# Performance work log

Measured on AMD Instinct MI355X. Metric: run time of the kernel, lower is better.

## Reference

```python
import jax, jax.numpy as jnp
import numpy as np

B, S, D, H = 32, 512, 768, 12
HD = D // H
FF = 4 * D
EPS = 1e-5


def layernorm(x, g, b):
    mu = jnp.mean(x, axis=-1, keepdims=True)
    var = jnp.mean(jnp.square(x - mu), axis=-1, keepdims=True)
    return (x - mu) * jax.lax.rsqrt(var + EPS) * g + b


def setup_inputs() -> dict:
    key = jax.random.key(0)
    ks = jax.random.split(key, 10)
    s = 0.02
    return {
        "x": jax.random.normal(ks[0], (B, S, D), jnp.float32),
        "edge_bias": jax.random.normal(ks[1], (H, S, S), jnp.float32) * s,
        "ln1_g": jnp.ones((D,), jnp.float32),
        "ln1_b": jnp.zeros((D,), jnp.float32),
        "qkv_w": jax.random.normal(ks[2], (3 * D, D), jnp.float32) * s,
        "qkv_b": jnp.zeros((3 * D,), jnp.float32),
        "proj_w": jax.random.normal(ks[3], (D, D), jnp.float32) * s,
        "proj_b": jnp.zeros((D,), jnp.float32),
        "ln2_g": jnp.ones((D,), jnp.float32),
        "ln2_b": jnp.zeros((D,), jnp.float32),
        "fc1_w": jax.random.normal(ks[4], (FF, D), jnp.float32) * s,
        "fc1_b": jnp.zeros((FF,), jnp.float32),
        "fc2_w": jax.random.normal(ks[5], (D, FF), jnp.float32) * s,
        "fc2_b": jnp.zeros((D,), jnp.float32),
    }


def reference(x, edge_bias, ln1_g, ln1_b, qkv_w, qkv_b, proj_w, proj_b,
              ln2_g, ln2_b, fc1_w, fc1_b, fc2_w, fc2_b):
    shortcut = x
    xn = layernorm(x, ln1_g, ln1_b)
    # qkv: [B,S,3D] -> [3,B,H,S,HD]
    qkv = (xn @ qkv_w.T + qkv_b).reshape(B, S, 3, H, HD).transpose(2, 0, 3, 1, 4)
    q, k, v = qkv[0], qkv[1], qkv[2]
    q = q * (HD ** -0.5)
    attn = jnp.einsum('bhqd,bhkd->bhqk', q, k) + edge_bias[None]
    attn = jax.nn.softmax(attn, axis=-1)
    o = jnp.einsum('bhqk,bhkd->bhqd', attn, v)
    o = o.transpose(0, 2, 1, 3).reshape(B, S, D)
    o = o @ proj_w.T + proj_b
    x = shortcut + o
    h = layernorm(x, ln2_g, ln2_b)
    h = jax.nn.gelu(h @ fc1_w.T + fc1_b, approximate=False)
    h = h @ fc2_w.T + fc2_b
    return x + h
```

## Files before the change

kernel.cpp:

```cpp
#include <hip/hip_runtime.h>

typedef unsigned short u16;
typedef unsigned int u32;
typedef float f32x4 __attribute__((ext_vector_type(4)));
typedef __bf16 bf16x8 __attribute__((ext_vector_type(8)));

__device__ __forceinline__ u16 f2bf(float f) {
  u32 u = __float_as_uint(f);
  u += 0x7fffu + ((u >> 16) & 1u);
  return (u16)(u >> 16);
}

__device__ __forceinline__ float bf2f(u16 v) {
  return __uint_as_float((u32)v << 16);
}

__device__ __forceinline__ void gload16(const u16* g, u16* l) {
  __builtin_amdgcn_global_load_lds(
      (__attribute__((address_space(1))) void*)(u16*)g,
      (__attribute__((address_space(3))) void*)l, 16, 0, 0);
}

__global__ __launch_bounds__(256) void cvt_bf16(const float* __restrict__ in,
                                                u16* __restrict__ o, int n4) {
  int i = blockIdx.x * 256 + threadIdx.x;
  if (i >= n4) return;
  float4 f = reinterpret_cast<const float4*>(in)[i];
  u32 lo = (u32)f2bf(f.x) | ((u32)f2bf(f.y) << 16);
  u32 hi = (u32)f2bf(f.z) | ((u32)f2bf(f.w) << 16);
  reinterpret_cast<uint2*>(o)[i] = make_uint2(lo, hi);
}

__global__ __launch_bounds__(256) void cvt_w_pack(const float* __restrict__ in,
                                                  u16* __restrict__ o, int N, int K) {
  int i = blockIdx.x * 256 + threadIdx.x;
  const int ng = K >> 3;
  if (i >= N * ng) return;
  const int n = i / ng;
  const int k = (i - n * ng) * 8;
  const float4 f0 = reinterpret_cast<const float4*>(in + (size_t)n * K + k)[0];
  const float4 f1 = reinterpret_cast<const float4*>(in + (size_t)n * K + k)[1];
  u32 p0 = (u32)f2bf(f0.x) | ((u32)f2bf(f0.y) << 16);
  u32 p1 = (u32)f2bf(f0.z) | ((u32)f2bf(f0.w) << 16);
  u32 p2 = (u32)f2bf(f1.x) | ((u32)f2bf(f1.y) << 16);
  u32 p3 = (u32)f2bf(f1.z) | ((u32)f2bf(f1.w) << 16);
  u16* dst = o + ((size_t)(k >> 5) * N + n) * 32 + (k & 31);
  reinterpret_cast<uint4*>(dst)[0] = make_uint4(p0, p1, p2, p3);
}

__global__ __launch_bounds__(256) void ln_bf16(const float* __restrict__ x,
                                               const float* __restrict__ g,
                                               const float* __restrict__ b,
                                               u16* __restrict__ o) {
  const int row = blockIdx.x;
  const int t = threadIdx.x;
  const float* xr = x + (size_t)row * 768;
  float a0 = xr[t], a1 = xr[t + 256], a2 = xr[t + 512];
  float s = a0 + a1 + a2;
  float ss = a0 * a0 + a1 * a1 + a2 * a2;
#pragma unroll
  for (int m = 1; m < 64; m <<= 1) {
    s += __shfl_xor(s, m);
    ss += __shfl_xor(ss, m);
  }
  __shared__ float sb[8];
  if ((t & 63) == 0) { sb[t >> 6] = s; sb[4 + (t >> 6)] = ss; }
  __syncthreads();
  s = sb[0] + sb[1] + sb[2] + sb[3];
  ss = sb[4] + sb[5] + sb[6] + sb[7];
  const float mu = s * (1.0f / 768.0f);
  const float var = ss * (1.0f / 768.0f) - mu * mu;
  const float rs = rsqrtf(var + 1e-5f);
#pragma unroll
  for (int c = 0; c < 3; ++c) {
    const int col = t + c * 256;
    const float a = (c == 0) ? a0 : (c == 1) ? a1 : a2;
    o[((size_t)(col >> 5) * 16384 + row) * 32 + (col & 31)] =
        f2bf((a - mu) * rs * g[col] + b[col]);
  }
}

enum { EPI_QKV = 0, EPI_PROJ = 1, EPI_GELU = 2, EPI_OUT = 3 };

template <int EPI>
__global__ __launch_bounds__(512, 2) void gemm_bt(
    const u16* __restrict__ A, const u16* __restrict__ W,
    const float* __restrict__ bias, const float* __restrict__ res,
    float* __restrict__ outf, u16* __restrict__ outb,
    u16* __restrict__ outq, u16* __restrict__ outk, u16* __restrict__ outv,
    int M, int N, int K) {
  __shared__ u16 SA[4 * 8192];
  __shared__ u16 SB[4 * 8192];
  const int tid = threadIdx.x;
  const int wid = tid >> 6, l = tid & 63;
  const int wm = wid >> 2, wn = wid & 3;
  const int lg = l >> 4, lc = l & 15;

  const u32 nbn = gridDim.x;
  const u32 orig = blockIdx.y * nbn + blockIdx.x;
  const u32 cpx = (nbn * gridDim.y) >> 3;
  const u32 wgid = (orig & 7) * cpx + (orig >> 3);
  const int bn = wgid % nbn;
  const int bm = wgid / nbn;

  const size_t Msl = (size_t)M * 32;
  const size_t Nsl = (size_t)N * 32;
  const size_t lane_a = (size_t)(bm * 256 + wid * 16 + (l >> 2)) * 32 +
                        (((l & 3) ^ ((l >> 3) & 3)) << 3);
  const size_t lane_w = (size_t)(bn * 256 + wid * 16 + (l >> 2)) * 32 +
                        (((l & 3) ^ ((l >> 3) & 3)) << 3);

  const int sg = (lg ^ ((lc >> 1) & 3)) << 3;

  f32x4 acc[8][4] = {};

  const int NU = K >> 5;

#define STAGE(u)                                                      \
  {                                                                   \
    const int slot_ = (u) & 3;                                        \
    const u16* Au_ = A + (size_t)(u) * Msl + lane_a;                  \
    const u16* Wu_ = W + (size_t)(u) * Nsl + lane_w;                  \
    gload16(Au_, &SA[slot_ * 8192 + wid * 512]);                      \
    gload16(Au_ + 4096, &SA[slot_ * 8192 + 4096 + wid * 512]);        \
    gload16(Wu_, &SB[slot_ * 8192 + wid * 512]);                      \
    gload16(Wu_ + 4096, &SB[slot_ * 8192 + 4096 + wid * 512]);        \
  }

  STAGE(0);
  STAGE(1);
  STAGE(2);
  asm volatile("s_waitcnt vmcnt(8)" ::: "memory");
  __builtin_amdgcn_s_barrier();

  for (int u = 0; u < NU; ++u) {
    const u16* sa = &SA[(u & 3) * 8192];
    const u16* sb = &SB[(u & 3) * 8192];
    bf16x8 af[8], bf[4];
#pragma unroll
    for (int mi = 0; mi < 8; ++mi)
      af[mi] = *reinterpret_cast<const bf16x8*>(&sa[(wm * 128 + mi * 16 + lc) * 32 + sg]);
#pragma unroll
    for (int ni = 0; ni < 4; ++ni)
      bf[ni] = *reinterpret_cast<const bf16x8*>(&sb[(wn * 64 + ni * 16 + lc) * 32 + sg]);
    if (u + 3 < NU) STAGE(u + 3);
    __builtin_amdgcn_s_barrier();
    __builtin_amdgcn_s_setprio(1);
#pragma unroll
    for (int mi = 0; mi < 8; ++mi)
#pragma unroll
      for (int ni = 0; ni < 4; ++ni)
        acc[mi][ni] = __builtin_amdgcn_mfma_f32_16x16x32_bf16(af[mi], bf[ni], acc[mi][ni], 0, 0, 0);
    __builtin_amdgcn_s_setprio(0);
    if (u + 3 < NU) {
      asm volatile("s_waitcnt vmcnt(8)" ::: "memory");
    } else if (u + 2 < NU) {
      asm volatile("s_waitcnt vmcnt(4)" ::: "memory");
    } else if (u + 1 < NU) {
      asm volatile("s_waitcnt vmcnt(0)" ::: "memory");
    }
    __builtin_amdgcn_s_barrier();
  }
#undef STAGE

  const int rbase = bm * 256 + wm * 128;
  const int cbase = bn * 256 + wn * 64;
#pragma unroll
  for (int mi = 0; mi < 8; ++mi) {
#pragma unroll
    for (int ni = 0; ni < 4; ++ni) {
#pragma unroll
      for (int r = 0; r < 4; ++r) {
        const int i = rbase + mi * 16 + lg * 4 + r;
        const int j = cbase + ni * 16 + lc;
        float v = acc[mi][ni][r] + bias[j];
        if constexpr (EPI == EPI_QKV) {
          const int t = j / 768;
          const int rr = j - t * 768;
          const int h = rr >> 6, hd = rr & 63;
          const int bb = i >> 9, ssi = i & 511;
          if (t == 0) {
            outq[((size_t)(bb * 12 + h) * 512 + ssi) * 64 + hd] = f2bf(v * 0.125f);
          } else if (t == 1) {
            outk[((size_t)(bb * 12 + h) * 512 + ssi) * 64 + hd] = f2bf(v);
          } else {
            outv[((size_t)(bb * 12 + h) * 64 + hd) * 512 + ssi] = f2bf(v);
          }
        } else if constexpr (EPI == EPI_PROJ) {
          outf[(size_t)i * 768 + j] = v + res[(size_t)i * 768 + j];
        } else if constexpr (EPI == EPI_GELU) {
          float gl = 0.5f * v * (1.0f + erff(v * 0.70710678118654752f));
          outb[((size_t)(j >> 5) * 16384 + i) * 32 + (j & 31)] = f2bf(gl);
        } else {
          outf[(size_t)i * 768 + j] = v + res[(size_t)i * 768 + j];
        }
      }
    }
  }
}

__global__ __launch_bounds__(256) void attn_fwd(const u16* __restrict__ q,
                                                const u16* __restrict__ k,
                                                const u16* __restrict__ vt,
                                                const u16* __restrict__ ebb,
                                                u16* __restrict__ o) {
  __shared__ u16 Ks[128 * 64];
  __shared__ u16 Vs[64 * 128];
  __shared__ u16 Bs[64 * 128];
  __shared__ u16 P[4 * 1024];
  const int tid = threadIdx.x;
  const int w = tid >> 6, l = tid & 63;
  const int lg = l >> 4, lc = l & 15;
  const int xcd = blockIdx.x & 7;
  const int wg = xcd * 384 + (blockIdx.x >> 3);
  const int qt = wg & 7;
  const int b = (wg >> 3) & 31;
  const int h = wg >> 8;
  const int bh = b * 12 + h;
  const int q0 = qt * 64;
  const u16* qp = q + (size_t)bh * 512 * 64;
  const u16* kp = k + (size_t)bh * 512 * 64;
  const u16* vtp = vt + (size_t)bh * 64 * 512;
  const u16* ep = ebb + (size_t)h * 262144 + (size_t)q0 * 512;

  bf16x8 aq[2];
#pragma unroll
  for (int kk = 0; kk < 2; ++kk)
    aq[kk] = *reinterpret_cast<const bf16x8*>(qp + (q0 + w * 16 + lc) * 64 + kk * 32 + lg * 8);

  float m[4], lsum[4];
  f32x4 oa[4] = {};
#pragma unroll
  for (int r = 0; r < 4; ++r) { m[r] = -1e30f; lsum[r] = 0.f; }

  const int krow_l = l >> 3;
  const int kgr = ((l & 7) ^ (l >> 3)) << 3;
  const int vrow_l = l >> 4;
  const int vswz = 4 * (w & 1) + (l >> 4);
  const int vgr = (((l & 15) ^ vswz)) << 3;
  const int bgr = (l & 15) << 3;
  char* Pw = (char*)&P[w * 1024];

  for (int kc = 0; kc < 4; ++kc) {
    const int kb = kc * 128;
    __syncthreads();
#pragma unroll
    for (int i = 0; i < 4; ++i) {
      const int grp = i * 4 + w;
      gload16(kp + (size_t)(kb + grp * 8 + krow_l) * 64 + kgr, &Ks[grp * 512]);
      gload16(vtp + (size_t)(grp * 4 + vrow_l) * 512 + kb + vgr, &Vs[grp * 512]);
      gload16(ep + (size_t)(grp * 4 + vrow_l) * 512 + kb + bgr, &Bs[grp * 512]);
    }
    __syncthreads();

    f32x4 s[8] = {};
#pragma unroll
    for (int kt = 0; kt < 8; ++kt) {
      const int kbyte = (kt * 16 + lc) * 128;
      const int sw = lc & 7;
      bf16x8 b0 = *reinterpret_cast<const bf16x8*>((const char*)Ks + kbyte + ((lg ^ sw) << 4));
      bf16x8 b1 = *reinterpret_cast<const bf16x8*>((const char*)Ks + kbyte + (((4 + lg) ^ sw) << 4));
      s[kt] = __builtin_amdgcn_mfma_f32_16x16x32_bf16(aq[0], b0, s[kt], 0, 0, 0);
      s[kt] = __builtin_amdgcn_mfma_f32_16x16x32_bf16(aq[1], b1, s[kt], 0, 0, 0);
    }
#pragma unroll
    for (int kt = 0; kt < 8; ++kt)
#pragma unroll
      for (int r = 0; r < 4; ++r)
        s[kt][r] += bf2f(Bs[(w * 16 + lg * 4 + r) * 128 + kt * 16 + lc]);
#pragma unroll
    for (int r = 0; r < 4; ++r) {
      float mc = s[0][r];
#pragma unroll
      for (int kt = 1; kt < 8; ++kt) mc = fmaxf(mc, s[kt][r]);
      mc = fmaxf(mc, __shfl_xor(mc, 1));
      mc = fmaxf(mc, __shfl_xor(mc, 2));
      mc = fmaxf(mc, __shfl_xor(mc, 4));
      mc = fmaxf(mc, __shfl_xor(mc, 8));
      const float mn = fmaxf(m[r], mc);
      const float al = __expf(m[r] - mn);
      m[r] = mn;
      float sum = 0.f;
#pragma unroll
      for (int kt = 0; kt < 8; ++kt) {
        float pv = __expf(s[kt][r] - mn);
        s[kt][r] = pv;
        sum += pv;
      }
      sum += __shfl_xor(sum, 1);
      sum += __shfl_xor(sum, 2);
      sum += __shfl_xor(sum, 4);
      sum += __shfl_xor(sum, 8);
      lsum[r] = lsum[r] * al + sum;
#pragma unroll
      for (int ni = 0; ni < 4; ++ni) oa[ni][r] *= al;
    }
#pragma unroll
    for (int kt = 0; kt < 8; ++kt)
#pragma unroll
      for (int r = 0; r < 4; ++r) {
        const int row = lg * 4 + r;
        int byte = (row << 8) + ((kt * 16 + lc) << 1);
        byte ^= (row & 7) << 4;
        *reinterpret_cast<u16*>(Pw + byte) = f2bf(s[kt][r]);
      }
#pragma unroll
    for (int ks = 0; ks < 4; ++ks) {
      int pbyte = (lc << 8) + ks * 64 + lg * 16;
      pbyte ^= (lc & 7) << 4;
      bf16x8 pa = *reinterpret_cast<const bf16x8*>(Pw + pbyte);
#pragma unroll
      for (int ni = 0; ni < 4; ++ni) {
        const int vbyte = (ni * 16 + lc) * 256 + (((ks * 4 + lg) ^ (lc & 7)) << 4);
        bf16x8 bv = *reinterpret_cast<const bf16x8*>((const char*)Vs + vbyte);
        oa[ni] = __builtin_amdgcn_mfma_f32_16x16x32_bf16(pa, bv, oa[ni], 0, 0, 0);
      }
    }
  }

  float inv[4];
#pragma unroll
  for (int r = 0; r < 4; ++r) inv[r] = 1.0f / lsum[r];
#pragma unroll
  for (int ni = 0; ni < 4; ++ni)
#pragma unroll
    for (int r = 0; r < 4; ++r) {
      const int i = b * 512 + q0 + w * 16 + lg * 4 + r;
      const int j = h * 64 + ni * 16 + lc;
      o[((size_t)(j >> 5) * 16384 + i) * 32 + (j & 31)] = f2bf(oa[ni][r] * inv[r]);
    }
}

extern "C" void kernel_launch(void* const* d_in, const int* in_sizes, int n_in,
                              void* d_out, int out_size, void* d_ws, size_t ws_size,
                              hipStream_t stream) {
  const float* x     = (const float*)d_in[0];
  const float* ebias = (const float*)d_in[1];
  const float* ln1g  = (const float*)d_in[2];
  const float* ln1b  = (const float*)d_in[3];
  const float* qkvw  = (const float*)d_in[4];
  const float* qkvb  = (const float*)d_in[5];
  const float* projw = (const float*)d_in[6];
  const float* projb = (const float*)d_in[7];
  const float* ln2g  = (const float*)d_in[8];
  const float* ln2b  = (const float*)d_in[9];
  const float* fc1w  = (const float*)d_in[10];
  const float* fc1b  = (const float*)d_in[11];
  const float* fc2w  = (const float*)d_in[12];
  const float* fc2b  = (const float*)d_in[13];
  float* out = (float*)d_out;

  char* p = (char*)d_ws;
  const size_t ACT = (size_t)16384 * 768 * 2;
  u16* xnb = (u16*)(p);
  u16* qb  = (u16*)(p + ACT);
  u16* kb  = (u16*)(p + 2 * ACT);
  u16* vb  = (u16*)(p + 3 * ACT);
  u16* ffb = (u16*)(p + 4 * ACT);
  u16* ebb = (u16*)(p + 4 * ACT);
  float* x2 = (float*)(p + 4 * ACT + (size_t)16384 * 3072 * 2);
  char* wz = p + 4 * ACT + (size_t)16384 * 3072 * 2 + (size_t)16384 * 768 * 4;
  u16* wq  = (u16*)wz;
  u16* wp  = wq + (size_t)2304 * 768;
  u16* wf1 = wp + (size_t)768 * 768;
  u16* wf2 = wf1 + (size_t)3072 * 768;

  cvt_w_pack<<<864, 256, 0, stream>>>(qkvw, wq, 2304, 768);
  cvt_w_pack<<<288, 256, 0, stream>>>(projw, wp, 768, 768);
  cvt_w_pack<<<1152, 256, 0, stream>>>(fc1w, wf1, 3072, 768);
  cvt_w_pack<<<1152, 256, 0, stream>>>(fc2w, wf2, 768, 3072);
  cvt_bf16<<<3072, 256, 0, stream>>>(ebias, ebb, 786432);

  ln_bf16<<<16384, 256, 0, stream>>>(x, ln1g, ln1b, xnb);

  gemm_bt<EPI_QKV><<<dim3(9, 64), 512, 0, stream>>>(
      xnb, wq, qkvb, nullptr, nullptr, nullptr, qb, kb, vb, 16384, 2304, 768);

  attn_fwd<<<3072, 256, 0, stream>>>(qb, kb, vb, ebb, xnb);

  gemm_bt<EPI_PROJ><<<dim3(3, 64), 512, 0, stream>>>(
      xnb, wp, projb, x, x2, nullptr, nullptr, nullptr, nullptr, 16384, 768, 768);

  ln_bf16<<<16384, 256, 0, stream>>>(x2, ln2g, ln2b, kb);

  gemm_bt<EPI_GELU><<<dim3(12, 64), 512, 0, stream>>>(
      kb, wf1, fc1b, nullptr, nullptr, ffb, nullptr, nullptr, nullptr, 16384, 3072, 768);

  gemm_bt<EPI_OUT><<<dim3(3, 64), 512, 0, stream>>>(
      ffb, wf2, fc2b, x2, out, nullptr, nullptr, nullptr, nullptr, 16384, 768, 3072);
}
```

Measured before the change: 536.9 us.

## Split GEMM main loop into two half-phases and use tanh-approx GELU

The GEMM k-loop is split into two phases. Each phase loads half of the A fragments, issues either the A or the W prefetch for stage u+3, and runs half of the MFMAs, with an extra barrier in between. The aim is to interleave global loads and LDS reads with MFMA work so the memory pipe and the matrix units overlap more. The exact erf GELU in the FC1 epilogue is also replaced by the tanh approximation written as a sigmoid with fast exp and rcp. This changes numerics slightly and may go beyond what the reference tolerance allows.

```diff
diff --git a/kernel.cpp b/kernel.cpp
--- a/kernel.cpp
+++ b/kernel.cpp
@@ -116,20 +116,24 @@
 
   const int NU = K >> 5;
 
-#define STAGE(u)                                                      \
+#define STAGE_A(u)                                                    \
   {                                                                   \
     const int slot_ = (u) & 3;                                        \
     const u16* Au_ = A + (size_t)(u) * Msl + lane_a;                  \
-    const u16* Wu_ = W + (size_t)(u) * Nsl + lane_w;                  \
     gload16(Au_, &SA[slot_ * 8192 + wid * 512]);                      \
     gload16(Au_ + 4096, &SA[slot_ * 8192 + 4096 + wid * 512]);        \
+  }
+#define STAGE_W(u)                                                    \
+  {                                                                   \
+    const int slot_ = (u) & 3;                                        \
+    const u16* Wu_ = W + (size_t)(u) * Nsl + lane_w;                  \
     gload16(Wu_, &SB[slot_ * 8192 + wid * 512]);                      \
     gload16(Wu_ + 4096, &SB[slot_ * 8192 + 4096 + wid * 512]);        \
   }
 
-  STAGE(0);
-  STAGE(1);
-  STAGE(2);
+  STAGE_A(0); STAGE_W(0);
+  STAGE_A(1); STAGE_W(1);
+  STAGE_A(2); STAGE_W(2);
   asm volatile("s_waitcnt vmcnt(8)" ::: "memory");
   __builtin_amdgcn_s_barrier();
 
@@ -138,16 +142,29 @@
     const u16* sb = &SB[(u & 3) * 8192];
     bf16x8 af[8], bf[4];
 #pragma unroll
-    for (int mi = 0; mi < 8; ++mi)
+    for (int mi = 0; mi < 4; ++mi)
       af[mi] = *reinterpret_cast<const bf16x8*>(&sa[(wm * 128 + mi * 16 + lc) * 32 + sg]);
 #pragma unroll
     for (int ni = 0; ni < 4; ++ni)
       bf[ni] = *reinterpret_cast<const bf16x8*>(&sb[(wn * 64 + ni * 16 + lc) * 32 + sg]);
-    if (u + 3 < NU) STAGE(u + 3);
+    if (u + 3 < NU) STAGE_A(u + 3);
     __builtin_amdgcn_s_barrier();
     __builtin_amdgcn_s_setprio(1);
 #pragma unroll
-    for (int mi = 0; mi < 8; ++mi)
+    for (int mi = 0; mi < 4; ++mi)
+#pragma unroll
+      for (int ni = 0; ni < 4; ++ni)
+        acc[mi][ni] = __builtin_amdgcn_mfma_f32_16x16x32_bf16(af[mi], bf[ni], acc[mi][ni], 0, 0, 0);
+    __builtin_amdgcn_s_setprio(0);
+    __builtin_amdgcn_s_barrier();
+#pragma unroll
+    for (int mi = 4; mi < 8; ++mi)
+      af[mi] = *reinterpret_cast<const bf16x8*>(&sa[(wm * 128 + mi * 16 + lc) * 32 + sg]);
+    if (u + 3 < NU) STAGE_W(u + 3);
+    __builtin_amdgcn_s_barrier();
+    __builtin_amdgcn_s_setprio(1);
+#pragma unroll
+    for (int mi = 4; mi < 8; ++mi)
 #pragma unroll
       for (int ni = 0; ni < 4; ++ni)
         acc[mi][ni] = __builtin_amdgcn_mfma_f32_16x16x32_bf16(af[mi], bf[ni], acc[mi][ni], 0, 0, 0);
@@ -161,7 +178,8 @@
     }
     __builtin_amdgcn_s_barrier();
   }
-#undef STAGE
+#undef STAGE_A
+#undef STAGE_W
 
   const int rbase = bm * 256 + wm * 128;
   const int cbase = bn * 256 + wn * 64;
@@ -189,7 +207,8 @@
         } else if constexpr (EPI == EPI_PROJ) {
           outf[(size_t)i * 768 + j] = v + res[(size_t)i * 768 + j];
         } else if constexpr (EPI == EPI_GELU) {
-          float gl = 0.5f * v * (1.0f + erff(v * 0.70710678118654752f));
+          float z = -1.5957691216f * v - 0.07135481627f * v * v * v;
+          float gl = v * __builtin_amdgcn_rcpf(1.0f + __expf(z));
           outb[((size_t)(j >> 5) * 16384 + i) * 32 + (j & 31)] = f2bf(gl);
         } else {
           outf[(size_t)i * 768 + j] = v + res[(size_t)i * 768 + j];
```

Result: no change. 534.4 us (-0.5%).

## Shrink GEMM tiles to 128x128 with double buffering and use sigmoid-GELU approximation

Applied to the files above, without the earlier changes.

Replaces the 256x256-tile, 512-thread, 4-stage-pipelined GEMM with a 128x128-tile, 256-thread, double-buffered version. It drops the explicit vmcnt waits and priority hints, and grids are doubled in each dimension. The exact erf GELU is also swapped for a tanh-style sigmoid approximation using fast exp and rcp. Smaller tiles mean less data reuse per block and a shallower pipeline. The GELU change alters numerics slightly.

```diff
diff --git a/kernel.cpp b/kernel.cpp
--- a/kernel.cpp
+++ b/kernel.cpp
@@ -83,17 +83,17 @@
 enum { EPI_QKV = 0, EPI_PROJ = 1, EPI_GELU = 2, EPI_OUT = 3 };
 
 template <int EPI>
-__global__ __launch_bounds__(512, 2) void gemm_bt(
+__global__ __launch_bounds__(256) void gemm_bt(
     const u16* __restrict__ A, const u16* __restrict__ W,
     const float* __restrict__ bias, const float* __restrict__ res,
     float* __restrict__ outf, u16* __restrict__ outb,
     u16* __restrict__ outq, u16* __restrict__ outk, u16* __restrict__ outv,
     int M, int N, int K) {
-  __shared__ u16 SA[4 * 8192];
-  __shared__ u16 SB[4 * 8192];
+  __shared__ u16 SA[2][128 * 32];
+  __shared__ u16 SB[2][128 * 32];
   const int tid = threadIdx.x;
   const int wid = tid >> 6, l = tid & 63;
-  const int wm = wid >> 2, wn = wid & 3;
+  const int wr = wid >> 1, wc = wid & 1;
   const int lg = l >> 4, lc = l & 15;
 
   const u32 nbn = gridDim.x;
@@ -105,68 +105,53 @@
 
   const size_t Msl = (size_t)M * 32;
   const size_t Nsl = (size_t)N * 32;
-  const size_t lane_a = (size_t)(bm * 256 + wid * 16 + (l >> 2)) * 32 +
+  const size_t lane_a = (size_t)(bm * 128 + wid * 16 + (l >> 2)) * 32 +
                         (((l & 3) ^ ((l >> 3) & 3)) << 3);
-  const size_t lane_w = (size_t)(bn * 256 + wid * 16 + (l >> 2)) * 32 +
+  const size_t lane_w = (size_t)(bn * 128 + wid * 16 + (l >> 2)) * 32 +
                         (((l & 3) ^ ((l >> 3) & 3)) << 3);
-
   const int sg = (lg ^ ((lc >> 1) & 3)) << 3;
 
-  f32x4 acc[8][4] = {};
+  f32x4 acc[4][4] = {};
 
   const int NU = K >> 5;
 
-#define STAGE(u)                                                      \
-  {                                                                   \
-    const int slot_ = (u) & 3;                                        \
-    const u16* Au_ = A + (size_t)(u) * Msl + lane_a;                  \
-    const u16* Wu_ = W + (size_t)(u) * Nsl + lane_w;                  \
-    gload16(Au_, &SA[slot_ * 8192 + wid * 512]);                      \
-    gload16(Au_ + 4096, &SA[slot_ * 8192 + 4096 + wid * 512]);        \
-    gload16(Wu_, &SB[slot_ * 8192 + wid * 512]);                      \
-    gload16(Wu_ + 4096, &SB[slot_ * 8192 + 4096 + wid * 512]);        \
-  }
-
-  STAGE(0);
-  STAGE(1);
-  STAGE(2);
-  asm volatile("s_waitcnt vmcnt(8)" ::: "memory");
-  __builtin_amdgcn_s_barrier();
-
+#define STAGE(u, buf)                                             \
+  {                                                               \
+    const u16* Au_ = A + (size_t)(u) * Msl + lane_a;              \
+    const u16* Wu_ = W + (size_t)(u) * Nsl + lane_w;              \
+    gload16(Au_, &SA[buf][wid * 512]);                            \
+    gload16(Au_ + 2048, &SA[buf][2048 + wid * 512]);              \
+    gload16(Wu_, &SB[buf][wid * 512]);                            \
+    gload16(Wu_ + 2048, &SB[buf][2048 + wid * 512]);              \
+  }
+
+  STAGE(0, 0);
+  __syncthreads();
+
+  int cur = 0;
   for (int u = 0; u < NU; ++u) {
-    const u16* sa = &SA[(u & 3) * 8192];
-    const u16* sb = &SB[(u & 3) * 8192];
-    bf16x8 af[8], bf[4];
-#pragma unroll
-    for (int mi = 0; mi < 8; ++mi)
-      af[mi] = *reinterpret_cast<const bf16x8*>(&sa[(wm * 128 + mi * 16 + lc) * 32 + sg]);
+    if (u + 1 < NU) STAGE(u + 1, cur ^ 1);
+    bf16x8 af[4], bf[4];
+#pragma unroll
+    for (int mi = 0; mi < 4; ++mi)
+      af[mi] = *reinterpret_cast<const bf16x8*>(&SA[cur][(wr * 64 + mi * 16 + lc) * 32 + sg]);
 #pragma unroll
     for (int ni = 0; ni < 4; ++ni)
-      bf[ni] = *reinterpret_cast<const bf16x8*>(&sb[(wn * 64 + ni * 16 + lc) * 32 + sg]);
-    if (u + 3 < NU) STAGE(u + 3);
-    __builtin_amdgcn_s_barrier();
-    __builtin_amdgcn_s_setprio(1);
-#pragma unroll
-    for (int mi = 0; mi < 8; ++mi)
+      bf[ni] = *reinterpret_cast<const bf16x8*>(&SB[cur][(wc * 64 + ni * 16 + lc) * 32 + sg]);
+#pragma unroll
+    for (int mi = 0; mi < 4; ++mi)
 #pragma unroll
       for (int ni = 0; ni < 4; ++ni)
         acc[mi][ni] = __builtin_amdgcn_mfma_f32_16x16x32_bf16(af[mi], bf[ni], acc[mi][ni], 0, 0, 0);
-    __builtin_amdgcn_s_setprio(0);
-    if (u + 3 < NU) {
-      asm volatile("s_waitcnt vmcnt(8)" ::: "memory");
-    } else if (u + 2 < NU) {
-      asm volatile("s_waitcnt vmcnt(4)" ::: "memory");
-    } else if (u + 1 < NU) {
-      asm volatile("s_waitcnt vmcnt(0)" ::: "memory");
-    }
-    __builtin_amdgcn_s_barrier();
+    __syncthreads();
+    cur ^= 1;
   }
 #undef STAGE
 
-  const int rbase = bm * 256 + wm * 128;
-  const int cbase = bn * 256 + wn * 64;
-#pragma unroll
-  for (int mi = 0; mi < 8; ++mi) {
+  const int rbase = bm * 128 + wr * 64;
+  const int cbase = bn * 128 + wc * 64;
+#pragma unroll
+  for (int mi = 0; mi < 4; ++mi) {
 #pragma unroll
     for (int ni = 0; ni < 4; ++ni) {
 #pragma unroll
@@ -189,7 +174,8 @@
         } else if constexpr (EPI == EPI_PROJ) {
           outf[(size_t)i * 768 + j] = v + res[(size_t)i * 768 + j];
         } else if constexpr (EPI == EPI_GELU) {
-          float gl = 0.5f * v * (1.0f + erff(v * 0.70710678118654752f));
+          float z = -1.5957691216f * v - 0.07135481627f * v * v * v;
+          float gl = v * __builtin_amdgcn_rcpf(1.0f + __expf(z));
           outb[((size_t)(j >> 5) * 16384 + i) * 32 + (j & 31)] = f2bf(gl);
         } else {
           outf[(size_t)i * 768 + j] = v + res[(size_t)i * 768 + j];
@@ -373,19 +359,19 @@
 
   ln_bf16<<<16384, 256, 0, stream>>>(x, ln1g, ln1b, xnb);
 
-  gemm_bt<EPI_QKV><<<dim3(9, 64), 512, 0, stream>>>(
+  gemm_bt<EPI_QKV><<<dim3(18, 128), 256, 0, stream>>>(
       xnb, wq, qkvb, nullptr, nullptr, nullptr, qb, kb, vb, 16384, 2304, 768);
 
   attn_fwd<<<3072, 256, 0, stream>>>(qb, kb, vb, ebb, xnb);
 
-  gemm_bt<EPI_PROJ><<<dim3(3, 64), 512, 0, stream>>>(
+  gemm_bt<EPI_PROJ><<<dim3(6, 128), 256, 0, stream>>>(
       xnb, wp, projb, x, x2, nullptr, nullptr, nullptr, nullptr, 16384, 768, 768);
 
   ln_bf16<<<16384, 256, 0, stream>>>(x2, ln2g, ln2b, kb);
 
-  gemm_bt<EPI_GELU><<<dim3(12, 64), 512, 0, stream>>>(
+  gemm_bt<EPI_GELU><<<dim3(24, 128), 256, 0, stream>>>(
       kb, wf1, fc1b, nullptr, nullptr, ffb, nullptr, nullptr, nullptr, 16384, 3072, 768);
 
-  gemm_bt<EPI_OUT><<<dim3(3, 64), 512, 0, stream>>>(
+  gemm_bt<EPI_OUT><<<dim3(6, 128), 256, 0, stream>>>(
       ffb, wf2, fc2b, x2, out, nullptr, nullptr, nullptr, nullptr, 16384, 768, 3072);
 }
```

Measured after the change: 599.3 us. 11.6% more time.

## Switch GEMM to double-buffered K=64 stages and use fast GELU approximation

Applied to the files above, without the earlier changes.

Restructures the GEMM main loop from a four-slot K=32 ring with three stages in flight to a two-slot double buffer holding K=64 per stage, with one block per CU. It aims to cut barriers and waitcnt overhead per K step. In exchange it reduces prefetch depth and occupancy, which can expose global load latency. The exact erf GELU in the fc1 epilogue is also replaced by a sigmoid-based tanh approximation using fast exp and reciprocal, which changes numerics slightly.

```diff
diff --git a/kernel.cpp b/kernel.cpp
--- a/kernel.cpp
+++ b/kernel.cpp
@@ -83,14 +83,14 @@
 enum { EPI_QKV = 0, EPI_PROJ = 1, EPI_GELU = 2, EPI_OUT = 3 };
 
 template <int EPI>
-__global__ __launch_bounds__(512, 2) void gemm_bt(
+__global__ __launch_bounds__(512, 1) void gemm_bt(
     const u16* __restrict__ A, const u16* __restrict__ W,
     const float* __restrict__ bias, const float* __restrict__ res,
     float* __restrict__ outf, u16* __restrict__ outb,
     u16* __restrict__ outq, u16* __restrict__ outk, u16* __restrict__ outv,
     int M, int N, int K) {
-  __shared__ u16 SA[4 * 8192];
-  __shared__ u16 SB[4 * 8192];
+  __shared__ u16 SA[2 * 16384];
+  __shared__ u16 SB[2 * 16384];
   const int tid = threadIdx.x;
   const int wid = tid >> 6, l = tid & 63;
   const int wm = wid >> 2, wn = wid & 3;
@@ -109,56 +109,57 @@
                         (((l & 3) ^ ((l >> 3) & 3)) << 3);
   const size_t lane_w = (size_t)(bn * 256 + wid * 16 + (l >> 2)) * 32 +
                         (((l & 3) ^ ((l >> 3) & 3)) << 3);
-
   const int sg = (lg ^ ((lc >> 1) & 3)) << 3;
 
   f32x4 acc[8][4] = {};
 
-  const int NU = K >> 5;
-
-#define STAGE(u)                                                      \
-  {                                                                   \
-    const int slot_ = (u) & 3;                                        \
-    const u16* Au_ = A + (size_t)(u) * Msl + lane_a;                  \
-    const u16* Wu_ = W + (size_t)(u) * Nsl + lane_w;                  \
-    gload16(Au_, &SA[slot_ * 8192 + wid * 512]);                      \
-    gload16(Au_ + 4096, &SA[slot_ * 8192 + 4096 + wid * 512]);        \
-    gload16(Wu_, &SB[slot_ * 8192 + wid * 512]);                      \
-    gload16(Wu_ + 4096, &SB[slot_ * 8192 + 4096 + wid * 512]);        \
-  }
-
-  STAGE(0);
-  STAGE(1);
-  STAGE(2);
-  asm volatile("s_waitcnt vmcnt(8)" ::: "memory");
+  const int NU = K >> 6;
+
+#define STAGE(u, slot)                                                  \
+  {                                                                     \
+    const u16* Au0_ = A + (size_t)(2 * (u)) * Msl + lane_a;             \
+    const u16* Au1_ = A + (size_t)(2 * (u) + 1) * Msl + lane_a;         \
+    const u16* Wu0_ = W + (size_t)(2 * (u)) * Nsl + lane_w;             \
+    const u16* Wu1_ = W + (size_t)(2 * (u) + 1) * Nsl + lane_w;         \
+    gload16(Au0_, &SA[(slot) * 16384 + wid * 512]);                     \
+    gload16(Au0_ + 4096, &SA[(slot) * 16384 + 4096 + wid * 512]);       \
+    gload16(Au1_, &SA[(slot) * 16384 + 8192 + wid * 512]);              \
+    gload16(Au1_ + 4096, &SA[(slot) * 16384 + 12288 + wid * 512]);      \
+    gload16(Wu0_, &SB[(slot) * 16384 + wid * 512]);                     \
+    gload16(Wu0_ + 4096, &SB[(slot) * 16384 + 4096 + wid * 512]);       \
+    gload16(Wu1_, &SB[(slot) * 16384 + 8192 + wid * 512]);              \
+    gload16(Wu1_ + 4096, &SB[(slot) * 16384 + 12288 + wid * 512]);      \
+  }
+
+  STAGE(0, 0);
+  asm volatile("s_waitcnt vmcnt(0)" ::: "memory");
   __builtin_amdgcn_s_barrier();
 
   for (int u = 0; u < NU; ++u) {
-    const u16* sa = &SA[(u & 3) * 8192];
-    const u16* sb = &SB[(u & 3) * 8192];
+    const int slot = u & 1;
+    if (u + 1 < NU) STAGE(u + 1, slot ^ 1);
+    const u16* sa = &SA[slot * 16384];
+    const u16* sb = &SB[slot * 16384];
     bf16x8 af[8], bf[4];
 #pragma unroll
-    for (int mi = 0; mi < 8; ++mi)
-      af[mi] = *reinterpret_cast<const bf16x8*>(&sa[(wm * 128 + mi * 16 + lc) * 32 + sg]);
-#pragma unroll
-    for (int ni = 0; ni < 4; ++ni)
-      bf[ni] = *reinterpret_cast<const bf16x8*>(&sb[(wn * 64 + ni * 16 + lc) * 32 + sg]);
-    if (u + 3 < NU) STAGE(u + 3);
-    __builtin_amdgcn_s_barrier();
-    __builtin_amdgcn_s_setprio(1);
-#pragma unroll
-    for (int mi = 0; mi < 8; ++mi)
+    for (int h = 0; h < 2; ++h) {
+#pragma unroll
+      for (int mi = 0; mi < 8; ++mi)
+        af[mi] = *reinterpret_cast<const bf16x8*>(
+            &sa[h * 8192 + (wm * 128 + mi * 16 + lc) * 32 + sg]);
 #pragma unroll
       for (int ni = 0; ni < 4; ++ni)
-        acc[mi][ni] = __builtin_amdgcn_mfma_f32_16x16x32_bf16(af[mi], bf[ni], acc[mi][ni], 0, 0, 0);
-    __builtin_amdgcn_s_setprio(0);
-    if (u + 3 < NU) {
-      asm volatile("s_waitcnt vmcnt(8)" ::: "memory");
-    } else if (u + 2 < NU) {
-      asm volatile("s_waitcnt vmcnt(4)" ::: "memory");
-    } else if (u + 1 < NU) {
-      asm volatile("s_waitcnt vmcnt(0)" ::: "memory");
-    }
+        bf[ni] = *reinterpret_cast<const bf16x8*>(
+            &sb[h * 8192 + (wn * 64 + ni * 16 + lc) * 32 + sg]);
+      __builtin_amdgcn_s_setprio(1);
+#pragma unroll
+      for (int mi = 0; mi < 8; ++mi)
+#pragma unroll
+        for (int ni = 0; ni < 4; ++ni)
+          acc[mi][ni] = __builtin_amdgcn_mfma_f32_16x16x32_bf16(af[mi], bf[ni], acc[mi][ni], 0, 0, 0);
+      __builtin_amdgcn_s_setprio(0);
+    }
+    asm volatile("s_waitcnt vmcnt(0)" ::: "memory");
     __builtin_amdgcn_s_barrier();
   }
 #undef STAGE
@@ -189,7 +190,8 @@
         } else if constexpr (EPI == EPI_PROJ) {
           outf[(size_t)i * 768 + j] = v + res[(size_t)i * 768 + j];
         } else if constexpr (EPI == EPI_GELU) {
-          float gl = 0.5f * v * (1.0f + erff(v * 0.70710678118654752f));
+          float z = -1.5957691216f * v - 0.07135481627f * v * v * v;
+          float gl = v * __builtin_amdgcn_rcpf(1.0f + __expf(z));
           outb[((size_t)(j >> 5) * 16384 + i) * 32 + (j & 31)] = f2bf(gl);
         } else {
           outf[(size_t)i * 768 + j] = v + res[(size_t)i * 768 + j];
```

New measurement: 546.9 us. Within noise of the previous version (+1.9%).
